# Kernel tuning notes

Hardware: AMD Instinct MI355X
Metric: run time of the kernel (lower is better)

Reference implementation:

```python
import jax, jax.numpy as jnp
import numpy as np

B, T, C = 8, 512, 512
H, HKV, D = 8, 4, 64
S_MAX = 128
BASE_FREQ = 10000.0
INIT_SIGMA = 256.0
EPS = 1e-6


def _init_positional_kernel(n_heads, head_dim, s_max, base_freq):
    table_size = 2 * s_max + 1
    deltas = jnp.arange(table_size) - s_max
    d_half = head_dim // 2
    freqs = 1.0 / base_freq ** (jnp.arange(d_half, dtype=jnp.float32) / d_half)
    phases = deltas[:, None].astype(jnp.float32) * freqs[None, :]
    P_single = jnp.concatenate([jnp.cos(phases), jnp.sin(phases)], axis=-1)
    return jnp.tile(P_single[None, :, :], (n_heads, 1, 1))


def setup_inputs() -> dict:
    key = jax.random.key(0)
    ks = jax.random.split(key, 6)
    scale = 0.02
    x = jax.random.normal(ks[0], (B, T, C), dtype=jnp.float32)
    Wq = jax.random.normal(ks[1], (C, H * D), dtype=jnp.float32) * scale
    Wk = jax.random.normal(ks[2], (C, HKV * D), dtype=jnp.float32) * scale
    Wv = jax.random.normal(ks[3], (C, HKV * D), dtype=jnp.float32) * scale
    Wproj = jax.random.normal(ks[4], (C, C), dtype=jnp.float32) * scale
    P = _init_positional_kernel(H, D, S_MAX, BASE_FREQ)
    sigma = jnp.full((H,), INIT_SIGMA, dtype=jnp.float32)
    return {"x": x, "Wq": Wq, "Wk": Wk, "Wv": Wv, "Wproj": Wproj, "P": P, "sigma": sigma}


def _norm(t):
    # nGPT-style: unit norm * sqrt(dim)
    dim = t.shape[-1]
    return t * (jnp.sqrt(float(dim)) * jax.lax.rsqrt((t * t).sum(axis=-1, keepdims=True) + EPS))


def _warped_kernel(P, sigma, T_):
    # P: [H, 2*S_MAX+1, D], sigma: [H] -> P_interp: [H, T, T, D]
    positions = jnp.arange(T_)
    delta = positions[:, None] - positions[None, :]  # [T, T]
    s = jnp.abs(sigma) + 1e-6
    delta_warped = S_MAX * jnp.tanh(delta[None, :, :].astype(jnp.float32) / s[:, None, None])
    delta_table = delta_warped + S_MAX  # [H, T, T]
    idx_lo = jnp.floor(delta_table).astype(jnp.int32)
    idx_hi = idx_lo + 1
    frac = delta_table - idx_lo.astype(P.dtype)
    table_max = 2 * S_MAX
    idx_lo = jnp.clip(idx_lo, 0, table_max)
    idx_hi = jnp.clip(idx_hi, 0, table_max)
    head_idx = jnp.arange(H)[:, None, None]
    P_lo = P[head_idx, idx_lo, :]  # [H, T, T, D]
    P_hi = P[head_idx, idx_hi, :]
    return (1 - frac[..., None]) * P_lo + frac[..., None] * P_hi


def reference(x, Wq, Wk, Wv, Wproj, P, sigma):
    q = (x @ Wq).reshape(B, T, H, D)
    k = (x @ Wk).reshape(B, T, HKV, D)
    v = (x @ Wv).reshape(B, T, HKV, D)
    q, k = _norm(q), _norm(k)
    repeats = H // HKV
    k = jnp.repeat(k, repeats, axis=2)
    v = jnp.repeat(v, repeats, axis=2)
    q = q.transpose(0, 2, 1, 3)  # [B, H, T, D]
    k = k.transpose(0, 2, 1, 3)
    v = v.transpose(0, 2, 1, 3)

    sm_scale = 1.0 / jnp.sqrt(float(D))
    P_interp = _warped_kernel(P, sigma, T)  # [H, T, T, D]
    S = jnp.einsum('bhid,hijd,bhjd->bhij', q, P_interp, k) * sm_scale
    causal_mask = jnp.tril(jnp.ones((T, T), dtype=jnp.bool_))
    S = jnp.where(causal_mask[None, None, :, :], S, jnp.finfo(S.dtype).min)
    A = jax.nn.softmax(S, axis=-1)
    y = A @ v  # [B, H, T, D]
    y = y.transpose(0, 2, 1, 3).reshape(B, T, H * D)
    return y @ Wproj
```

## Files before the change

### kernel.cpp

```cpp
#include <hip/hip_runtime.h>
#include <hip/hip_bf16.h>
#include <math.h>

#define Bb 8
#define Tt 512
#define Cc 512
#define Hh 8
#define HKV 4
#define Dd 64

typedef __attribute__((ext_vector_type(8))) short short8;
typedef __attribute__((ext_vector_type(4))) float float4v;
typedef __attribute__((ext_vector_type(2))) __fp16 h2;
typedef __attribute__((ext_vector_type(8))) __fp16 half8;

__device__ __forceinline__ h2 u2h(unsigned u) {
  union { unsigned u; h2 h; } x; x.u = u; return x.h;
}
__device__ __forceinline__ unsigned h2u(h2 h) {
  union { h2 h; unsigned u; } x; x.h = h; return x.u;
}
__device__ __forceinline__ float fdot2(h2 a, h2 b, float c) {
#if __has_builtin(__builtin_amdgcn_fdot2)
  return __builtin_amdgcn_fdot2(a, b, c, false);
#else
  return fmaf((float)a.x, (float)b.x, fmaf((float)a.y, (float)b.y, c));
#endif
}

__device__ __forceinline__ float wave_reduce_sum(float v) {
#pragma unroll
  for (int off = 32; off > 0; off >>= 1) v += __shfl_xor(v, off, 64);
  return v;
}
__device__ __forceinline__ unsigned pack_bf2(float a, float b) {
  __hip_bfloat162 h = __float22bfloat162_rn(make_float2(a, b));
  return *(unsigned*)&h;
}

__global__ __launch_bounds__(256) void prep(
    const float* __restrict__ x, const float* __restrict__ Wq,
    const float* __restrict__ Wk, const float* __restrict__ Wv,
    const float* __restrict__ Wp, const float* __restrict__ P,
    const float* __restrict__ sigma,
    unsigned short* __restrict__ xb, unsigned short* __restrict__ Wtq,
    unsigned short* __restrict__ Wtp, unsigned short* __restrict__ Pwh) {
  const int bid = blockIdx.x;
  const int t = threadIdx.x;
  if (bid < 1024) {
    int i = (bid * 256 + t) * 8;
    float4 f0 = *(const float4*)&x[i];
    float4 f1 = *(const float4*)&x[i + 4];
    unsigned u[4] = {pack_bf2(f0.x, f0.y), pack_bf2(f0.z, f0.w),
                     pack_bf2(f1.x, f1.y), pack_bf2(f1.z, f1.w)};
    *(uint4*)&xb[i] = *(uint4*)u;
  } else if (bid < 1216) {
    __shared__ float Ts[64][65];
    const int bx = bid - 1024;
    const int k0 = (bx & 7) << 6;
    const int n0 = (bx >> 3) << 6;
    const float* src; int ld, nc0; unsigned short* dst; int ndst;
    if (n0 < 512)       { src = Wq; ld = 512; nc0 = n0;        dst = Wtq; ndst = n0; }
    else if (n0 < 768)  { src = Wk; ld = 256; nc0 = n0 - 512;  dst = Wtq; ndst = n0; }
    else if (n0 < 1024) { src = Wv; ld = 256; nc0 = n0 - 768;  dst = Wtq; ndst = n0; }
    else                { src = Wp; ld = 512; nc0 = n0 - 1024; dst = Wtp; ndst = n0 - 1024; }
    const int r = t >> 4, c4 = (t & 15) << 2;
#pragma unroll
    for (int rr = 0; rr < 4; ++rr) {
      int row = (rr << 4) + r;
      float4 f = *(const float4*)&src[(k0 + row) * ld + nc0 + c4];
      Ts[row][c4] = f.x; Ts[row][c4 + 1] = f.y;
      Ts[row][c4 + 2] = f.z; Ts[row][c4 + 3] = f.w;
    }
    __syncthreads();
#pragma unroll
    for (int rr = 0; rr < 4; ++rr) {
      int nr = (rr << 4) + r;
      unsigned u0 = pack_bf2(Ts[c4][nr], Ts[c4 + 1][nr]);
      unsigned u1 = pack_bf2(Ts[c4 + 2][nr], Ts[c4 + 3][nr]);
      *(uint2*)&dst[(ndst + nr) * 512 + k0 + c4] = make_uint2(u0, u1);
    }
  } else {
    int idx = (bid - 1216) * 256 + t;
    int d = idx & 63;
    int rem = idx >> 6;
    int dd = rem % 1023;
    int h = rem / 1023;
    float s = fabsf(sigma[h]) + 1e-6f;
    float delta = (float)(dd - 511);
    float dt = 128.0f * tanhf(delta / s) + 128.0f;
    float lo = floorf(dt);
    int ilo = (int)lo;
    float frac = dt - lo;
    ilo = max(0, min(ilo, 256));
    int ihi = min(ilo + 1, 256);
    const float* Pb = P + h * 257 * 64;
    float val = (1.0f - frac) * Pb[ilo * 64 + d] + frac * Pb[ihi * 64 + d];
    __fp16 hv = (__fp16)val;
    Pwh[idx] = *(unsigned short*)&hv;
  }
}

__global__ __launch_bounds__(256) void qkv_mfma(
    const unsigned short* __restrict__ xb, const unsigned short* __restrict__ Wt,
    unsigned short* __restrict__ qh, unsigned short* __restrict__ kh,
    unsigned short* __restrict__ vT) {
  __shared__ unsigned short As[64][72];
  __shared__ unsigned short Bs[64][72];
  const int m0 = blockIdx.x * 64;
  const int n0 = blockIdx.y * 64;
  const int t = threadIdx.x;
  const int w = t >> 6, lane = t & 63;
  const int srow = t >> 2, sc = (t & 3) << 4;
  float4v acc[4] = {{0,0,0,0},{0,0,0,0},{0,0,0,0},{0,0,0,0}};
  for (int k0 = 0; k0 < 512; k0 += 64) {
    uint4 a0 = *(const uint4*)&xb[(m0 + srow) * 512 + k0 + sc];
    uint4 a1 = *(const uint4*)&xb[(m0 + srow) * 512 + k0 + sc + 8];
    uint4 b0 = *(const uint4*)&Wt[(n0 + srow) * 512 + k0 + sc];
    uint4 b1 = *(const uint4*)&Wt[(n0 + srow) * 512 + k0 + sc + 8];
    __syncthreads();
    *(uint4*)&As[srow][sc] = a0; *(uint4*)&As[srow][sc + 8] = a1;
    *(uint4*)&Bs[srow][sc] = b0; *(uint4*)&Bs[srow][sc + 8] = b1;
    __syncthreads();
    const int ml = (w << 4) + (lane & 15);
    const int kq = (lane >> 4) << 3;
    short8 aF0 = *(short8*)&As[ml][kq];
    short8 aF1 = *(short8*)&As[ml][kq + 32];
#pragma unroll
    for (int nt = 0; nt < 4; ++nt) {
      const int nl = (nt << 4) + (lane & 15);
      short8 bF0 = *(short8*)&Bs[nl][kq];
      short8 bF1 = *(short8*)&Bs[nl][kq + 32];
      acc[nt] = __builtin_amdgcn_mfma_f32_16x16x32_bf16(aF0, bF0, acc[nt], 0, 0, 0);
      acc[nt] = __builtin_amdgcn_mfma_f32_16x16x32_bf16(aF1, bF1, acc[nt], 0, 0, 0);
    }
  }
  const int lane15 = lane & 15;
  const int rowbase = m0 + (w << 4) + ((lane >> 4) << 2);
  if (n0 < 768) {
#pragma unroll
    for (int r = 0; r < 4; ++r) {
      float ss = 0.0f;
#pragma unroll
      for (int nt = 0; nt < 4; ++nt) ss = fmaf(acc[nt][r], acc[nt][r], ss);
#pragma unroll
      for (int off = 1; off < 16; off <<= 1) ss += __shfl_xor(ss, off, 64);
      float sc2 = 8.0f * rsqrtf(ss + 1e-6f);
      const int row = rowbase + r;
      if (n0 < 512) {
        const int h = n0 >> 6;
#pragma unroll
        for (int nt = 0; nt < 4; ++nt) {
          __fp16 hv = (__fp16)(acc[nt][r] * sc2);
          qh[(row * Hh + h) * Dd + (nt << 4) + lane15] = *(unsigned short*)&hv;
        }
      } else {
        const int hkv = (n0 - 512) >> 6;
#pragma unroll
        for (int nt = 0; nt < 4; ++nt) {
          __fp16 hv = (__fp16)(acc[nt][r] * sc2);
          kh[(row * HKV + hkv) * Dd + (nt << 4) + lane15] = *(unsigned short*)&hv;
        }
      }
    }
  } else {
    const int hkv = (n0 - 768) >> 6;
    const int bb = rowbase >> 9;
    const int trow = rowbase & 511;
#pragma unroll
    for (int nt = 0; nt < 4; ++nt) {
      const int d = (nt << 4) + lane15;
      unsigned u0 = h2u(__builtin_amdgcn_cvt_pkrtz(acc[nt][0], acc[nt][1]));
      unsigned u1 = h2u(__builtin_amdgcn_cvt_pkrtz(acc[nt][2], acc[nt][3]));
      *(uint2*)&vT[((bb * HKV + hkv) * 64 + d) * 512 + trow] = make_uint2(u0, u1);
    }
  }
}

__global__ __launch_bounds__(256) void proj_mfma(
    const unsigned short* __restrict__ yb, const unsigned short* __restrict__ Wt,
    float* __restrict__ out) {
  __shared__ unsigned short As[64][72];
  __shared__ unsigned short Bs[64][72];
  const int m0 = blockIdx.x * 64;
  const int n0 = blockIdx.y * 64;
  const int t = threadIdx.x;
  const int w = t >> 6, lane = t & 63;
  const int srow = t >> 2, sc = (t & 3) << 4;
  float4v acc[4] = {{0,0,0,0},{0,0,0,0},{0,0,0,0},{0,0,0,0}};
  for (int k0 = 0; k0 < 512; k0 += 64) {
    uint4 a0 = *(const uint4*)&yb[(m0 + srow) * 512 + k0 + sc];
    uint4 a1 = *(const uint4*)&yb[(m0 + srow) * 512 + k0 + sc + 8];
    uint4 b0 = *(const uint4*)&Wt[(n0 + srow) * 512 + k0 + sc];
    uint4 b1 = *(const uint4*)&Wt[(n0 + srow) * 512 + k0 + sc + 8];
    __syncthreads();
    *(uint4*)&As[srow][sc] = a0; *(uint4*)&As[srow][sc + 8] = a1;
    *(uint4*)&Bs[srow][sc] = b0; *(uint4*)&Bs[srow][sc + 8] = b1;
    __syncthreads();
    const int ml = (w << 4) + (lane & 15);
    const int kq = (lane >> 4) << 3;
    short8 aF0 = *(short8*)&As[ml][kq];
    short8 aF1 = *(short8*)&As[ml][kq + 32];
#pragma unroll
    for (int nt = 0; nt < 4; ++nt) {
      const int nl = (nt << 4) + (lane & 15);
      short8 bF0 = *(short8*)&Bs[nl][kq];
      short8 bF1 = *(short8*)&Bs[nl][kq + 32];
      acc[nt] = __builtin_amdgcn_mfma_f32_16x16x32_bf16(aF0, bF0, acc[nt], 0, 0, 0);
      acc[nt] = __builtin_amdgcn_mfma_f32_16x16x32_bf16(aF1, bF1, acc[nt], 0, 0, 0);
    }
  }
#pragma unroll
  for (int nt = 0; nt < 4; ++nt) {
    int col = n0 + (nt << 4) + (lane & 15);
#pragma unroll
    for (int r = 0; r < 4; ++r) {
      int row = m0 + (w << 4) + ((lane >> 4) << 2) + r;
      out[row * 512 + col] = acc[nt][r];
    }
  }
}

__global__ __launch_bounds__(256) void attn(
    const unsigned short* __restrict__ qh, const unsigned short* __restrict__ kh,
    const unsigned short* __restrict__ vT, const unsigned short* __restrict__ Pwh,
    unsigned short* __restrict__ yb) {
  __shared__ __fp16 PwS[96][72];
  __shared__ __fp16 pS[32][72];
  __shared__ float lS[32];

  const int t = threadIdx.x;
  const int lane = t & 63;
  const int wu = __builtin_amdgcn_readfirstlane(t >> 6);
  const int bh = blockIdx.x;
  const int b = bh >> 3;
  const int h = bh & 7;
  const int hkv = h >> 1;
  const int i0 = 480 - blockIdx.y * 32;

  float l_lane[8];
#pragma unroll
  for (int r = 0; r < 8; ++r) l_lane[r] = 0.0f;
  float4v oacc[2] = {{0, 0, 0, 0}, {0, 0, 0, 0}};

  const int prow = (wu << 3) + 63 - lane;
  const int i_base = i0 + (wu << 3);
  const unsigned short* qbase = &qh[((b * Tt + i_base) * Hh + h) * Dd];

  const int i16 = (wu & 1) << 4;
  const int dt0 = (wu >> 1) << 1;
  const int lm = lane & 15;
  const int kq = (lane >> 4) << 3;
  const unsigned short* vTbase = &vT[((b * HKV + hkv) * 64) * 512];

  for (int jt0 = 0; jt0 <= i0 + 31; jt0 += 64) {
    __syncthreads();
    {
      int jr = t >> 2, dc = (t & 3) << 4;
      const int pb0 = h * 1023 + (i0 - jt0) + 448;
      const unsigned short* pwp = &Pwh[(pb0 + jr) * 64 + dc];
      *(uint4*)&PwS[jr][dc]     = *(const uint4*)&pwp[0];
      *(uint4*)&PwS[jr][dc + 8] = *(const uint4*)&pwp[8];
      int pr2 = 64 + (t >> 3), dc2 = (t & 7) << 3;
      if (pr2 < 95)
        *(uint4*)&PwS[pr2][dc2] = *(const uint4*)&Pwh[(pb0 + pr2) * 64 + dc2];
    }
    uint4 kr[8];
    {
      const uint4* kp = (const uint4*)&kh[((b * Tt + jt0 + lane) * HKV + hkv) * Dd];
#pragma unroll
      for (int c = 0; c < 8; ++c) kr[c] = kp[c];
    }
    __syncthreads();

    const int j = jt0 + lane;
#pragma unroll
    for (int r = 0; r < 8; ++r) {
      const uint4* qp = (const uint4*)&qbase[r * (Hh * Dd)];
      float sr = 0.0f;
#pragma unroll
      for (int ch = 0; ch < 8; ++ch) {
        uint4 qu = qp[ch];
        uint4 pu = *(uint4*)&PwS[prow + r][ch << 3];
        sr = fdot2(u2h(qu.x) * u2h(pu.x), u2h(kr[ch].x), sr);
        sr = fdot2(u2h(qu.y) * u2h(pu.y), u2h(kr[ch].y), sr);
        sr = fdot2(u2h(qu.z) * u2h(pu.z), u2h(kr[ch].z), sr);
        sr = fdot2(u2h(qu.w) * u2h(pu.w), u2h(kr[ch].w), sr);
      }
      float sv = (j <= i_base + r) ? sr * 0.125f : -1e30f;
      float p = __expf(sv - 6.0f);
      l_lane[r] += p;
      pS[(wu << 3) + r][lane] = (__fp16)p;
    }
    __syncthreads();

    half8 a0 = *(half8*)&pS[i16 + lm][kq];
    half8 a1 = *(half8*)&pS[i16 + lm][kq + 32];
#pragma unroll
    for (int dd = 0; dd < 2; ++dd) {
      const unsigned short* vp = vTbase + (((dt0 + dd) << 4) + lm) * 512 + jt0 + kq;
      half8 b0 = *(const half8*)&vp[0];
      half8 b1 = *(const half8*)&vp[32];
      oacc[dd] = __builtin_amdgcn_mfma_f32_16x16x32_f16(a0, b0, oacc[dd], 0, 0, 0);
      oacc[dd] = __builtin_amdgcn_mfma_f32_16x16x32_f16(a1, b1, oacc[dd], 0, 0, 0);
    }
  }

#pragma unroll
  for (int r = 0; r < 8; ++r) {
    float lr = wave_reduce_sum(l_lane[r]);
    if (lane == r) lS[(wu << 3) + r] = lr;
  }
  __syncthreads();

#pragma unroll
  for (int dd = 0; dd < 2; ++dd) {
    const int d = ((dt0 + dd) << 4) + lm;
#pragma unroll
    for (int r = 0; r < 4; ++r) {
      const int irow = i16 + ((lane >> 4) << 2) + r;
      const float val = oacc[dd][r] / lS[irow];
      __hip_bfloat16 hv = __float2bfloat16(val);
      yb[((b * Tt + i0 + irow) * Hh + h) * Dd + d] = *(unsigned short*)&hv;
    }
  }
}

extern "C" void kernel_launch(void* const* d_in, const int* in_sizes, int n_in,
                              void* d_out, int out_size, void* d_ws, size_t ws_size,
                              hipStream_t stream) {
  const float* x     = (const float*)d_in[0];
  const float* Wq    = (const float*)d_in[1];
  const float* Wk    = (const float*)d_in[2];
  const float* Wv    = (const float*)d_in[3];
  const float* Wproj = (const float*)d_in[4];
  const float* P     = (const float*)d_in[5];
  const float* sigma = (const float*)d_in[6];
  float* out = (float*)d_out;

  float* ws = (float*)d_ws;
  unsigned short* qh  = (unsigned short*)ws;
  unsigned short* kh  = (unsigned short*)(ws + 1048576);
  unsigned short* vT  = (unsigned short*)(ws + 1572864);
  unsigned short* Pwh = (unsigned short*)(ws + 2097152);
  unsigned short* xb  = (unsigned short*)(ws + 2359296);
  unsigned short* yb  = xb;
  unsigned short* Wtq = (unsigned short*)(ws + 3407872);
  unsigned short* Wtp = (unsigned short*)(ws + 3670016);

  prep<<<dim3(3262), 256, 0, stream>>>(x, Wq, Wk, Wv, Wproj, P, sigma,
                                       xb, Wtq, Wtp, Pwh);
  qkv_mfma<<<dim3(64, 16), 256, 0, stream>>>(xb, Wtq, qh, kh, vT);
  attn<<<dim3(64, 16), 256, 0, stream>>>(qh, kh, vT, Pwh, yb);
  proj_mfma<<<dim3(64, 8), 256, 0, stream>>>(yb, Wtp, out);
}
```

Baseline: 136.8 us.

## Fuse x bf16 conversion into QKV GEMM and read warped P directly from global

The separate pass that converts x to bf16 in the prep kernel is removed. The QKV GEMM now loads fp32 x and packs it to bf16 while staging tiles, which drops a full write and read of the converted activation buffer. Separately, the attention kernel no longer stages the warped positional table into shared memory with a barrier. Each lane instead reads its Pw rows directly from global/L2. This removes one __syncthreads and the LDS traffic, but the QKV GEMM now reads twice the bytes for x, once per N-tile, and P reads become uncoalesced global loads repeated across waves.

```diff
diff --git a/kernel.cpp b/kernel.cpp
--- a/kernel.cpp
+++ b/kernel.cpp
@@ -39,26 +39,17 @@
 }
 
 __global__ __launch_bounds__(256) void prep(
-    const float* __restrict__ x, const float* __restrict__ Wq,
-    const float* __restrict__ Wk, const float* __restrict__ Wv,
-    const float* __restrict__ Wp, const float* __restrict__ P,
-    const float* __restrict__ sigma,
-    unsigned short* __restrict__ xb, unsigned short* __restrict__ Wtq,
-    unsigned short* __restrict__ Wtp, unsigned short* __restrict__ Pwh) {
+    const float* __restrict__ Wq, const float* __restrict__ Wk,
+    const float* __restrict__ Wv, const float* __restrict__ Wp,
+    const float* __restrict__ P, const float* __restrict__ sigma,
+    unsigned short* __restrict__ Wtq, unsigned short* __restrict__ Wtp,
+    unsigned short* __restrict__ Pwh) {
   const int bid = blockIdx.x;
   const int t = threadIdx.x;
-  if (bid < 1024) {
-    int i = (bid * 256 + t) * 8;
-    float4 f0 = *(const float4*)&x[i];
-    float4 f1 = *(const float4*)&x[i + 4];
-    unsigned u[4] = {pack_bf2(f0.x, f0.y), pack_bf2(f0.z, f0.w),
-                     pack_bf2(f1.x, f1.y), pack_bf2(f1.z, f1.w)};
-    *(uint4*)&xb[i] = *(uint4*)u;
-  } else if (bid < 1216) {
+  if (bid < 192) {
     __shared__ float Ts[64][65];
-    const int bx = bid - 1024;
-    const int k0 = (bx & 7) << 6;
-    const int n0 = (bx >> 3) << 6;
+    const int k0 = (bid & 7) << 6;
+    const int n0 = (bid >> 3) << 6;
     const float* src; int ld, nc0; unsigned short* dst; int ndst;
     if (n0 < 512)       { src = Wq; ld = 512; nc0 = n0;        dst = Wtq; ndst = n0; }
     else if (n0 < 768)  { src = Wk; ld = 256; nc0 = n0 - 512;  dst = Wtq; ndst = n0; }
@@ -81,7 +72,8 @@
       *(uint2*)&dst[(ndst + nr) * 512 + k0 + c4] = make_uint2(u0, u1);
     }
   } else {
-    int idx = (bid - 1216) * 256 + t;
+    int idx = (bid - 192) * 256 + t;
+    if (idx >= Hh * 1023 * 64) return;
     int d = idx & 63;
     int rem = idx >> 6;
     int dd = rem % 1023;
@@ -102,7 +94,7 @@
 }
 
 __global__ __launch_bounds__(256) void qkv_mfma(
-    const unsigned short* __restrict__ xb, const unsigned short* __restrict__ Wt,
+    const float* __restrict__ x, const unsigned short* __restrict__ Wt,
     unsigned short* __restrict__ qh, unsigned short* __restrict__ kh,
     unsigned short* __restrict__ vT) {
   __shared__ unsigned short As[64][72];
@@ -114,12 +106,20 @@
   const int srow = t >> 2, sc = (t & 3) << 4;
   float4v acc[4] = {{0,0,0,0},{0,0,0,0},{0,0,0,0},{0,0,0,0}};
   for (int k0 = 0; k0 < 512; k0 += 64) {
-    uint4 a0 = *(const uint4*)&xb[(m0 + srow) * 512 + k0 + sc];
-    uint4 a1 = *(const uint4*)&xb[(m0 + srow) * 512 + k0 + sc + 8];
+    const float* xp = &x[(m0 + srow) * 512 + k0 + sc];
+    float4 f0 = *(const float4*)&xp[0];
+    float4 f1 = *(const float4*)&xp[4];
+    float4 f2 = *(const float4*)&xp[8];
+    float4 f3 = *(const float4*)&xp[12];
+    unsigned au[8] = {pack_bf2(f0.x, f0.y), pack_bf2(f0.z, f0.w),
+                      pack_bf2(f1.x, f1.y), pack_bf2(f1.z, f1.w),
+                      pack_bf2(f2.x, f2.y), pack_bf2(f2.z, f2.w),
+                      pack_bf2(f3.x, f3.y), pack_bf2(f3.z, f3.w)};
     uint4 b0 = *(const uint4*)&Wt[(n0 + srow) * 512 + k0 + sc];
     uint4 b1 = *(const uint4*)&Wt[(n0 + srow) * 512 + k0 + sc + 8];
     __syncthreads();
-    *(uint4*)&As[srow][sc] = a0; *(uint4*)&As[srow][sc + 8] = a1;
+    *(uint4*)&As[srow][sc] = *(uint4*)&au[0];
+    *(uint4*)&As[srow][sc + 8] = *(uint4*)&au[4];
     *(uint4*)&Bs[srow][sc] = b0; *(uint4*)&Bs[srow][sc + 8] = b1;
     __syncthreads();
     const int ml = (w << 4) + (lane & 15);
@@ -225,7 +225,6 @@
     const unsigned short* __restrict__ qh, const unsigned short* __restrict__ kh,
     const unsigned short* __restrict__ vT, const unsigned short* __restrict__ Pwh,
     unsigned short* __restrict__ yb) {
-  __shared__ __fp16 PwS[96][72];
   __shared__ __fp16 pS[32][72];
   __shared__ float lS[32];
 
@@ -254,34 +253,27 @@
   const unsigned short* vTbase = &vT[((b * HKV + hkv) * 64) * 512];
 
   for (int jt0 = 0; jt0 <= i0 + 31; jt0 += 64) {
-    __syncthreads();
-    {
-      int jr = t >> 2, dc = (t & 3) << 4;
-      const int pb0 = h * 1023 + (i0 - jt0) + 448;
-      const unsigned short* pwp = &Pwh[(pb0 + jr) * 64 + dc];
-      *(uint4*)&PwS[jr][dc]     = *(const uint4*)&pwp[0];
-      *(uint4*)&PwS[jr][dc + 8] = *(const uint4*)&pwp[8];
-      int pr2 = 64 + (t >> 3), dc2 = (t & 7) << 3;
-      if (pr2 < 95)
-        *(uint4*)&PwS[pr2][dc2] = *(const uint4*)&Pwh[(pb0 + pr2) * 64 + dc2];
-    }
     uint4 kr[8];
     {
       const uint4* kp = (const uint4*)&kh[((b * Tt + jt0 + lane) * HKV + hkv) * Dd];
 #pragma unroll
       for (int c = 0; c < 8; ++c) kr[c] = kp[c];
     }
+    const int pb0 = h * 1023 + (i0 - jt0) + 448;
+    const uint4* pwrow0 = (const uint4*)&Pwh[(pb0 + prow) * 64];
+
     __syncthreads();
 
     const int j = jt0 + lane;
 #pragma unroll
     for (int r = 0; r < 8; ++r) {
       const uint4* qp = (const uint4*)&qbase[r * (Hh * Dd)];
+      const uint4* pwp = pwrow0 + r * 8;
       float sr = 0.0f;
 #pragma unroll
       for (int ch = 0; ch < 8; ++ch) {
         uint4 qu = qp[ch];
-        uint4 pu = *(uint4*)&PwS[prow + r][ch << 3];
+        uint4 pu = pwp[ch];
         sr = fdot2(u2h(qu.x) * u2h(pu.x), u2h(kr[ch].x), sr);
         sr = fdot2(u2h(qu.y) * u2h(pu.y), u2h(kr[ch].y), sr);
         sr = fdot2(u2h(qu.z) * u2h(pu.z), u2h(kr[ch].z), sr);
@@ -343,14 +335,12 @@
   unsigned short* kh  = (unsigned short*)(ws + 1048576);
   unsigned short* vT  = (unsigned short*)(ws + 1572864);
   unsigned short* Pwh = (unsigned short*)(ws + 2097152);
-  unsigned short* xb  = (unsigned short*)(ws + 2359296);
-  unsigned short* yb  = xb;
+  unsigned short* yb  = (unsigned short*)(ws + 2359296);
   unsigned short* Wtq = (unsigned short*)(ws + 3407872);
   unsigned short* Wtp = (unsigned short*)(ws + 3670016);
 
-  prep<<<dim3(3262), 256, 0, stream>>>(x, Wq, Wk, Wv, Wproj, P, sigma,
-                                       xb, Wtq, Wtp, Pwh);
-  qkv_mfma<<<dim3(64, 16), 256, 0, stream>>>(xb, Wtq, qh, kh, vT);
+  prep<<<dim3(2238), 256, 0, stream>>>(Wq, Wk, Wv, Wproj, P, sigma, Wtq, Wtp, Pwh);
+  qkv_mfma<<<dim3(64, 16), 256, 0, stream>>>(x, Wtq, qh, kh, vT);
   attn<<<dim3(64, 16), 256, 0, stream>>>(qh, kh, vT, Pwh, yb);
   proj_mfma<<<dim3(64, 8), 256, 0, stream>>>(yb, Wtp, out);
 }
```

New measurement: 266.6 us. 94.9% more time.
